# Optimization experiments

Hardware: AMD Instinct MI355X
Metric: run time of the kernel (lower is better)

Reference implementation:

```python
import jax, jax.numpy as jnp
import numpy as np

H = 768
NH = 12
HD = H // NH
NDIM = 5
LN_EPS = 1e-5


def setup_inputs() -> dict:
    key = jax.random.key(0)
    ks = jax.random.split(key, 12)
    B, S = 4, 2048
    xavier = lambda k: jax.random.uniform(k, (H, H), jnp.float32, -1.0, 1.0) * np.sqrt(6.0 / (H + H))
    return {
        "hidden_states": jax.random.normal(ks[0], (B, S, H), jnp.float32),
        "Wq": xavier(ks[1]), "bq": jnp.zeros((H,), jnp.float32),
        "Wk": xavier(ks[2]), "bk": jnp.zeros((H,), jnp.float32),
        "Wv": xavier(ks[3]), "bv": jnp.zeros((H,), jnp.float32),
        "Wo": xavier(ks[4]), "bo": jnp.zeros((H,), jnp.float32),
        # per-dimension, per-head scalar biases (torch init: zeros; use small randn so grads are non-trivial)
        "dim_biases": 0.02 * jax.random.normal(ks[5], (NDIM, NH), jnp.float32),
        "ln_gamma": jnp.ones((H,), jnp.float32),
        "ln_beta": jnp.zeros((H,), jnp.float32),
        "attention_mask": jax.random.randint(ks[6], (4, 2048), 0, 2, jnp.int32),
        "dimension_idx": 2,
    }


def reference(hidden_states, Wq, bq, Wk, bk, Wv, bv, Wo, bo, dim_biases,
              ln_gamma, ln_beta, attention_mask, dimension_idx):
    B, S, _ = hidden_states.shape
    residual = hidden_states
    # torch nn.Linear: x @ W.T + b
    q = (hidden_states @ Wq.T + bq).reshape(B, S, NH, HD).transpose(0, 2, 1, 3)  # [B,NH,S,HD]
    k = (hidden_states @ Wk.T + bk).reshape(B, S, NH, HD).transpose(0, 2, 1, 3)
    v = (hidden_states @ Wv.T + bv).reshape(B, S, NH, HD).transpose(0, 2, 1, 3)

    scores = jnp.einsum("bhqd,bhkd->bhqk", q, k) / np.sqrt(HD)  # [B,NH,S,S]
    if dimension_idx is not None and dimension_idx < NDIM:
        scores = scores + dim_biases[dimension_idx][None, :, None, None]
    # mask over key positions, broadcast over heads and queries
    scores = jnp.where(attention_mask[:, None, None, :] == 0, -jnp.inf, scores)
    attn = jax.nn.softmax(scores, axis=-1)

    ctx = jnp.einsum("bhqk,bhkd->bhqd", attn, v)  # [B,NH,S,HD]
    ctx = ctx.transpose(0, 2, 1, 3).reshape(B, S, H)
    out = ctx @ Wo.T + bo

    y = out + residual
    mu = jnp.mean(y, axis=-1, keepdims=True)
    var = jnp.var(y, axis=-1, keepdims=True)
    y = (y - mu) / jnp.sqrt(var + LN_EPS) * ln_gamma + ln_beta
    return y
```

## Files before the change

kernel.cpp:

```cpp
#include <hip/hip_runtime.h>
#include <hip/hip_bf16.h>

#define HH    768
#define NHEAD 12
#define HDIM  64
#define BB    4
#define SS    2048
#define MM    (BB*SS)
#define NDIMS 5
#define WEL   (HH*HH)
#define LOG2E 1.44269504088896f
#define QSCALE 0.180336881f

typedef unsigned short u16;
typedef __attribute__((ext_vector_type(8))) short short8;
typedef __attribute__((ext_vector_type(4))) float floatx4;
typedef __attribute__((ext_vector_type(16))) float floatx16;
typedef __attribute__((ext_vector_type(4))) unsigned int uint4v;
typedef __attribute__((ext_vector_type(2))) unsigned int uint2v;

__device__ __forceinline__ float bf2f(u16 u) {
    return __uint_as_float(((unsigned int)u) << 16);
}
__device__ __forceinline__ u16 f2bf(float f) {
    unsigned int x = __float_as_uint(f);
    unsigned int r = (x + 0x7fffu + ((x >> 16) & 1u)) >> 16;
    return (u16)r;
}
__device__ __forceinline__ unsigned int pack_bf16x2(float a, float b) {
    float2 f2 = make_float2(a, b);
    __hip_bfloat162 h2 = __float22bfloat162_rn(f2);
    return *reinterpret_cast<unsigned int*>(&h2);
}
__device__ __forceinline__ void gld16(const u16* g, u16* l) {
    __builtin_amdgcn_global_load_lds(
        (const __attribute__((address_space(1))) unsigned int*)g,
        (__attribute__((address_space(3))) unsigned int*)l, 16, 0, 0);
}

__global__ __launch_bounds__(256) void f32_to_bf16(
    const float* __restrict__ in, u16* __restrict__ out, int n8)
{
    int i = blockIdx.x * 256 + threadIdx.x;
    if (i >= n8) return;
    float4 a = ((const float4*)in)[i*2];
    float4 b = ((const float4*)in)[i*2 + 1];
    ushort4 lo, hi;
    lo.x = f2bf(a.x); lo.y = f2bf(a.y); lo.z = f2bf(a.z); lo.w = f2bf(a.w);
    hi.x = f2bf(b.x); hi.y = f2bf(b.y); hi.z = f2bf(b.z); hi.w = f2bf(b.w);
    ((ushort4*)out)[i*2]     = lo;
    ((ushort4*)out)[i*2 + 1] = hi;
}

#define XCVT_BLKS ((MM*HH)/8/256)
#define WCVT_BLKS (WEL/8/256)
__global__ __launch_bounds__(256) void cvt_all(
    const float* __restrict__ x,
    const float* __restrict__ W0, const float* __restrict__ W1,
    const float* __restrict__ W2, const float* __restrict__ W3,
    u16* __restrict__ xb, u16* __restrict__ wb)
{
    const int bid = blockIdx.x;
    const float* src;
    u16* dst;
    int i;
    if (bid < XCVT_BLKS) {
        src = x; dst = xb; i = bid * 256 + threadIdx.x;
    } else {
        const int wsel = (bid - XCVT_BLKS) / WCVT_BLKS;
        src = (wsel == 0) ? W0 : (wsel == 1) ? W1 : (wsel == 2) ? W2 : W3;
        dst = wb + (size_t)wsel * WEL;
        i = ((bid - XCVT_BLKS) % WCVT_BLKS) * 256 + threadIdx.x;
    }
    float4 a = ((const float4*)src)[i*2];
    float4 b = ((const float4*)src)[i*2 + 1];
    ushort4 lo, hi;
    lo.x = f2bf(a.x); lo.y = f2bf(a.y); lo.z = f2bf(a.z); lo.w = f2bf(a.w);
    hi.x = f2bf(b.x); hi.y = f2bf(b.y); hi.z = f2bf(b.z); hi.w = f2bf(b.w);
    ((ushort4*)dst)[i*2]     = lo;
    ((ushort4*)dst)[i*2 + 1] = hi;
}

__global__ __launch_bounds__(256) void v_transpose(
    const u16* __restrict__ V, u16* __restrict__ vt)
{
    __shared__ unsigned Ls[64][36];
    const int t = threadIdx.x;
    const int kt = blockIdx.x, h = blockIdx.y, b = blockIdx.z;
    const int p  = t & 31;
    const int dg = (t >> 5) * 8;
    const u16* va = V + ((size_t)(b*SS + kt*64 + 2*p))*HH + h*HDIM + dg;
    const u16* vb = va + HH;
    uint4 A = *(const uint4*)va;
    uint4 Bv = *(const uint4*)vb;
    const unsigned* Aw = (const unsigned*)&A;
    const unsigned* Bw = (const unsigned*)&Bv;
    #pragma unroll
    for (int i = 0; i < 4; ++i) {
        unsigned a = Aw[i], c = Bw[i];
        Ls[dg + 2*i][p]     = (a & 0xffffu) | (c << 16);
        Ls[dg + 2*i + 1][p] = (a >> 16) | (c & 0xffff0000u);
    }
    __syncthreads();
    const int d = t >> 2, kc = (t & 3) * 8;
    uint4 o0 = *(const uint4*)&Ls[d][kc];
    uint4 o1 = *(const uint4*)&Ls[d][kc + 4];
    u16* dst = vt + ((size_t)((b*NHEAD + h)*HDIM + d))*SS + kt*64 + kc*2;
    *(uint4*)dst       = o0;
    *(uint4*)(dst + 8) = o1;
}

__global__ __launch_bounds__(256, 3) void gemm_gld_qkv(
    const u16* __restrict__ Xb, const u16* __restrict__ Wb3,
    const float* __restrict__ bq, const float* __restrict__ bk, const float* __restrict__ bv,
    u16* __restrict__ oq, u16* __restrict__ ok, u16* __restrict__ ov)
{
    __shared__ u16 Xs[128][64];
    __shared__ u16 Ws[192][64];
    const int t = threadIdx.x;
    const int w = t >> 6, lane = t & 63;
    const int wy = w >> 1, wx = w & 1;
    const int m = lane & 31, hh = lane >> 5;
    const int grow = lane >> 3;
    const int cg   = (lane & 7) ^ grow;

    const int flat = blockIdx.x + 12 * blockIdx.y;
    const int swz  = (flat & 7) * 96 + (flat >> 3);
    const int j0 = (swz % 12) * 192;
    const int i0 = (swz / 12) * 128;
    const int sel = j0 / HH;
    const int lj  = j0 - sel * HH;
    const float* biasL = ((sel == 0) ? bq : (sel == 1) ? bk : bv) + lj;
    u16* outL = ((sel == 0) ? oq : (sel == 1) ? ok : ov) + lj;
    const u16* Wrows = Wb3 + (size_t)j0 * HH;

    floatx16 acc[2][3];
    #pragma unroll
    for (int am = 0; am < 2; ++am)
        #pragma unroll
        for (int bn = 0; bn < 3; ++bn)
            #pragma unroll
            for (int r = 0; r < 16; ++r) acc[am][bn][r] = 0.f;

    for (int k0 = 0; k0 < HH; k0 += 64) {
        __syncthreads();
        #pragma unroll
        for (int j = 0; j < 4; ++j) {
            const int r = w*32 + j*8;
            gld16(Xb + (size_t)(i0 + r + grow)*HH + k0 + cg*8, &Xs[r][0]);
        }
        #pragma unroll
        for (int j = 0; j < 6; ++j) {
            const int r = w*48 + j*8;
            gld16(Wrows + (size_t)(r + grow)*HH + k0 + cg*8, &Ws[r][0]);
        }
        __syncthreads();

        #pragma unroll
        for (int kh = 0; kh < 4; ++kh) {
            const int ch = kh*2 + hh;
            short8 af[2], bf[3];
            #pragma unroll
            for (int am = 0; am < 2; ++am) {
                const int row = wy*64 + am*32 + m;
                af[am] = *(const short8*)&Xs[row][(ch ^ (m & 7))*8];
            }
            #pragma unroll
            for (int bn = 0; bn < 3; ++bn) {
                const int row = wx*96 + bn*32 + m;
                bf[bn] = *(const short8*)&Ws[row][(ch ^ (m & 7))*8];
            }
            #pragma unroll
            for (int am = 0; am < 2; ++am)
                #pragma unroll
                for (int bn = 0; bn < 3; ++bn)
                    acc[am][bn] = __builtin_amdgcn_mfma_f32_32x32x16_bf16(
                        af[am], bf[bn], acc[am][bn], 0, 0, 0);
        }
    }

    float bb[3];
    #pragma unroll
    for (int bn = 0; bn < 3; ++bn) bb[bn] = biasL[wx*96 + bn*32 + m];
    #pragma unroll
    for (int am = 0; am < 2; ++am)
        #pragma unroll
        for (int bn = 0; bn < 3; ++bn)
            #pragma unroll
            for (int r = 0; r < 16; ++r) {
                int row = i0 + wy*64 + am*32 + (r & 3) + 8*(r >> 2) + 4*hh;
                outL[(size_t)row*HH + wx*96 + bn*32 + m] = f2bf(acc[am][bn][r] + bb[bn]);
            }
}

__global__ __launch_bounds__(256) void gemm_gld_m64(
    const u16* __restrict__ Xb, const u16* __restrict__ Wb,
    const float* __restrict__ bias, u16* __restrict__ out)
{
    __shared__ u16 Xs[64][64];
    __shared__ u16 Ws[128][64];
    const int t = threadIdx.x;
    const int w = t >> 6, lane = t & 63;
    const int m = lane & 31, hh = lane >> 5;
    const int grow = lane >> 3;
    const int cg   = (lane & 7) ^ grow;

    const int flat = blockIdx.x + 6 * blockIdx.y;
    const int swz  = (flat & 7) * 96 + (flat >> 3);
    const int j0 = (swz % 6) * 128;
    const int i0 = (swz / 6) * 64;

    floatx16 acc[2];
    #pragma unroll
    for (int am = 0; am < 2; ++am)
        #pragma unroll
        for (int r = 0; r < 16; ++r) acc[am][r] = 0.f;

    for (int k0 = 0; k0 < HH; k0 += 64) {
        __syncthreads();
        #pragma unroll
        for (int j = 0; j < 2; ++j) {
            const int r = w*16 + j*8;
            gld16(Xb + (size_t)(i0 + r + grow)*HH + k0 + cg*8, &Xs[r][0]);
        }
        #pragma unroll
        for (int j = 0; j < 4; ++j) {
            const int r = w*32 + j*8;
            gld16(Wb + (size_t)(j0 + r + grow)*HH + k0 + cg*8, &Ws[r][0]);
        }
        __syncthreads();

        #pragma unroll
        for (int kh = 0; kh < 4; ++kh) {
            const int ch = kh*2 + hh;
            short8 af[2], bf;
            af[0] = *(const short8*)&Xs[m][(ch ^ (m & 7))*8];
            af[1] = *(const short8*)&Xs[32 + m][(ch ^ (m & 7))*8];
            bf    = *(const short8*)&Ws[w*32 + m][(ch ^ (m & 7))*8];
            acc[0] = __builtin_amdgcn_mfma_f32_32x32x16_bf16(af[0], bf, acc[0], 0, 0, 0);
            acc[1] = __builtin_amdgcn_mfma_f32_32x32x16_bf16(af[1], bf, acc[1], 0, 0, 0);
        }
    }

    const float bb = bias[j0 + w*32 + m];
    #pragma unroll
    for (int am = 0; am < 2; ++am)
        #pragma unroll
        for (int r = 0; r < 16; ++r) {
            int row = i0 + am*32 + (r & 3) + 8*(r >> 2) + 4*hh;
            out[(size_t)row*HH + j0 + w*32 + m] = f2bf(acc[am][r] + bb);
        }
}

__global__ __launch_bounds__(256) void gemm_mfma_nt(
    const u16* __restrict__ Xb, const float* __restrict__ W,
    const float* __restrict__ bias, u16* __restrict__ out)
{
    __shared__ u16 Xs[128][40];
    __shared__ u16 Wt[64][40];
    const int t = threadIdx.x;
    const int w = t >> 6, lane = t & 63;
    const int c = lane & 15, qd = lane >> 4;
    const int i0 = blockIdx.y * 128, j0 = blockIdx.x * 64;
    const int xrow = t >> 1, xoff = (t & 1) * 16;
    const int wn = t >> 2, woff = (t & 3) * 8;

    floatx4 acc[2][4];
    #pragma unroll
    for (int mt = 0; mt < 2; ++mt)
        #pragma unroll
        for (int nt = 0; nt < 4; ++nt) acc[mt][nt] = (floatx4){0.f,0.f,0.f,0.f};

    for (int k0 = 0; k0 < HH; k0 += 32) {
        uint4 xa  = *(const uint4*)(Xb + (size_t)(i0 + xrow)*HH + k0 + xoff);
        uint4 xb2 = *(const uint4*)(Xb + (size_t)(i0 + xrow)*HH + k0 + xoff + 8);
        float4 wa = *(const float4*)(W + (size_t)(j0 + wn)*HH + k0 + woff);
        float4 wb = *(const float4*)(W + (size_t)(j0 + wn)*HH + k0 + woff + 4);
        __syncthreads();
        *(uint4*)&Xs[xrow][xoff]     = xa;
        *(uint4*)&Xs[xrow][xoff + 8] = xb2;
        ushort4 w0, w1;
        w0.x = f2bf(wa.x); w0.y = f2bf(wa.y); w0.z = f2bf(wa.z); w0.w = f2bf(wa.w);
        w1.x = f2bf(wb.x); w1.y = f2bf(wb.y); w1.z = f2bf(wb.z); w1.w = f2bf(wb.w);
        *(ushort4*)&Wt[wn][woff]     = w0;
        *(ushort4*)&Wt[wn][woff + 4] = w1;
        __syncthreads();

        short8 a0 = *(const short8*)&Xs[w*32 + c][qd*8];
        short8 a1 = *(const short8*)&Xs[w*32 + 16 + c][qd*8];
        #pragma unroll
        for (int nt = 0; nt < 4; ++nt) {
            short8 bfr = *(const short8*)&Wt[nt*16 + c][qd*8];
            acc[0][nt] = __builtin_amdgcn_mfma_f32_16x16x32_bf16(a0, bfr, acc[0][nt], 0, 0, 0);
            acc[1][nt] = __builtin_amdgcn_mfma_f32_16x16x32_bf16(a1, bfr, acc[1][nt], 0, 0, 0);
        }
    }

    float bv[4];
    #pragma unroll
    for (int nt = 0; nt < 4; ++nt) bv[nt] = bias[j0 + nt*16 + c];
    #pragma unroll
    for (int mt = 0; mt < 2; ++mt)
        #pragma unroll
        for (int nt = 0; nt < 4; ++nt)
            #pragma unroll
            for (int r = 0; r < 4; ++r)
                out[(size_t)(i0 + w*32 + mt*16 + qd*4 + r)*HH + j0 + nt*16 + c] =
                    f2bf(acc[mt][nt][r] + bv[nt]);
}

__global__ __launch_bounds__(256, 3) void attn_mfma32(
    const u16* __restrict__ Q, const u16* __restrict__ K, const u16* __restrict__ vt,
    const float* __restrict__ dim_biases, const int* __restrict__ mask,
    const int* __restrict__ dim_idx_p, u16* __restrict__ ctx)
{
    __shared__ u16 Ks[2][64][64];
    __shared__ u16 Vs[2][64][64];
    __shared__ float madd[2][64];

    const int t = threadIdx.x;
    const int w = t >> 6, lane = t & 63;
    const int ql = lane & 31, hi = lane >> 5;
    const int sw7 = ql & 7;

    const int flat = blockIdx.x + 16 * (blockIdx.y + 12 * blockIdx.z);
    const int swz  = (flat & 7) * 96 + (flat >> 3);
    const int q0 = (swz & 15) * 128;
    const int h  = (swz >> 4) % NHEAD;
    const int b  = swz / (16 * NHEAD);

    const int didx = *dim_idx_p;
    const float db2 = ((didx < NDIMS) ? dim_biases[didx*NHEAD + h] : 0.f) * LOG2E;

    const int grow = lane >> 3;
    const int cg   = (lane & 7) ^ grow;

    const u16* Vrows = vt + (size_t)(b*NHEAD + h)*HDIM*SS;

    short8 ones;
    #pragma unroll
    for (int j = 0; j < 8; ++j) ones[j] = (short)0x3F80;

    short8 qv[4];
    {
        const u16* qsrc = Q + ((size_t)(b*SS + q0 + w*32 + ql))*HH + h*HDIM + 8*hi;
        #pragma unroll
        for (int s = 0; s < 4; ++s) {
            ushort4 u0 = *(const ushort4*)(qsrc + s*16);
            ushort4 u1 = *(const ushort4*)(qsrc + s*16 + 4);
            const u16 uu[8] = {u0.x,u0.y,u0.z,u0.w,u1.x,u1.y,u1.z,u1.w};
            #pragma unroll
            for (int j = 0; j < 8; ++j)
                qv[s][j] = (short)f2bf(bf2f(uu[j]) * QSCALE);
        }
    }

    floatx16 o[2], lacc;
    #pragma unroll
    for (int r = 0; r < 16; ++r) { o[0][r] = 0.f; o[1][r] = 0.f; lacc[r] = 0.f; }

    int mreg = 0;

    auto issueKV = [&](int kt, int buf) {
        #pragma unroll
        for (int j = 0; j < 2; ++j) {
            const int rbase = w*16 + j*8;
            gld16(K + (size_t)(b*SS + kt*64 + rbase + grow)*HH + h*HDIM + cg*8,
                  &Ks[buf][rbase][0]);
            gld16(Vrows + (size_t)(rbase + grow)*SS + kt*64 + cg*8,
                  &Vs[buf][rbase][0]);
        }
    };
    auto issueM = [&](int kt) {
        if (t < 64) mreg = mask[(size_t)b*SS + kt*64 + t];
    };
    auto writeM = [&](int buf) {
        if (t < 64) madd[buf][t] = (mreg != 0) ? db2 : -1e30f;
    };

    issueKV(0, 0);
    issueM(0);
    writeM(0);

    for (int kt = 0; kt < SS/64; ++kt) {
        const int cur = kt & 1;
        __syncthreads();
        const bool more = (kt + 1 < SS/64);
        if (more) { issueKV(kt + 1, cur ^ 1); issueM(kt + 1); }

        #pragma unroll
        for (int kblk = 0; kblk < 2; ++kblk) {
            const u16* kb = &Ks[cur][kblk*32 + ql][0];

            floatx16 z;
            #pragma unroll
            for (int qq = 0; qq < 4; ++qq) {
                float4 mv = *(const float4*)&madd[cur][kblk*32 + qq*8 + 4*hi];
                z[qq*4+0] = mv.x; z[qq*4+1] = mv.y; z[qq*4+2] = mv.z; z[qq*4+3] = mv.w;
            }
            short8 kf[4];
            #pragma unroll
            for (int s = 0; s < 4; ++s)
                kf[s] = *(const short8*)(kb + ((s*2 + hi) ^ sw7)*8);
            __builtin_amdgcn_s_setprio(1);
            #pragma unroll
            for (int s = 0; s < 4; ++s)
                z = __builtin_amdgcn_mfma_f32_32x32x16_bf16(kf[s], qv[s], z, 0, 0, 0);
            __builtin_amdgcn_s_setprio(0);

            #pragma unroll
            for (int r = 0; r < 16; ++r) z[r] = __builtin_amdgcn_exp2f(z[r]);

            #pragma unroll
            for (int ks = 0; ks < 2; ++ks) {
                unsigned x0 = pack_bf16x2(z[ks*8 + 0], z[ks*8 + 1]);
                unsigned y0 = pack_bf16x2(z[ks*8 + 4], z[ks*8 + 5]);
                unsigned x1 = pack_bf16x2(z[ks*8 + 2], z[ks*8 + 3]);
                unsigned y1 = pack_bf16x2(z[ks*8 + 6], z[ks*8 + 7]);
                uint2v s0 = __builtin_amdgcn_permlane32_swap(x0, y0, false, false);
                uint2v s1 = __builtin_amdgcn_permlane32_swap(x1, y1, false, false);
                uint4v pv; pv[0] = s0[0]; pv[1] = s1[0]; pv[2] = s0[1]; pv[3] = s1[1];
                short8 pa = __builtin_bit_cast(short8, pv);

                const int ck = kblk*4 + ks*2 + hi;
                short8 vf0 = *(const short8*)&Vs[cur][ql][(ck ^ sw7)*8];
                short8 vf1 = *(const short8*)&Vs[cur][32 + ql][(ck ^ sw7)*8];

                __builtin_amdgcn_s_setprio(1);
                lacc = __builtin_amdgcn_mfma_f32_32x32x16_bf16(pa, ones, lacc, 0, 0, 0);
                o[0] = __builtin_amdgcn_mfma_f32_32x32x16_bf16(pa, vf0, o[0], 0, 0, 0);
                o[1] = __builtin_amdgcn_mfma_f32_32x32x16_bf16(pa, vf1, o[1], 0, 0, 0);
                __builtin_amdgcn_s_setprio(0);
            }
        }

        if (more) writeM(cur ^ 1);
    }

    #pragma unroll
    for (int r = 0; r < 16; ++r) {
        float l = lacc[r];
        float inv = (l > 0.f) ? 1.f / l : 0.f;
        const int qrow = q0 + w*32 + (r & 3) + 8*(r >> 2) + 4*hi;
        u16* dst = ctx + ((size_t)(b*SS + qrow))*HH + h*HDIM + ql;
        dst[0]  = f2bf(o[0][r] * inv);
        dst[32] = f2bf(o[1][r] * inv);
    }
}

__global__ __launch_bounds__(256) void add_ln_wave(
    const u16* __restrict__ proj, const float* __restrict__ resid,
    const float* __restrict__ gamma, const float* __restrict__ beta,
    float* __restrict__ out)
{
    const int t = threadIdx.x, w = t >> 6, lane = t & 63;
    const int row = blockIdx.x * 4 + w;
    const size_t base = (size_t)row * HH + lane * 12;
    const int gbase = lane * 12;

    float x[12];
    #pragma unroll
    for (int j = 0; j < 3; ++j) {
        ushort4 p = *(const ushort4*)(proj + base + j*4);
        float4  r = *(const float4*)(resid + base + j*4);
        x[j*4+0] = bf2f(p.x) + r.x;
        x[j*4+1] = bf2f(p.y) + r.y;
        x[j*4+2] = bf2f(p.z) + r.z;
        x[j*4+3] = bf2f(p.w) + r.w;
    }
    float s = 0.f, ss = 0.f;
    #pragma unroll
    for (int j = 0; j < 12; ++j) { s += x[j]; ss += x[j]*x[j]; }
    #pragma unroll
    for (int off = 1; off < 64; off <<= 1) {
        s  += __shfl_xor(s, off);
        ss += __shfl_xor(ss, off);
    }
    float mean = s * (1.f/768.f);
    float var  = ss * (1.f/768.f) - mean*mean;
    float rstd = rsqrtf(fmaxf(var, 0.f) + 1e-5f);
    #pragma unroll
    for (int j = 0; j < 3; ++j) {
        float4 g = *(const float4*)(gamma + gbase + j*4);
        float4 bt = *(const float4*)(beta + gbase + j*4);
        float4 y;
        y.x = (x[j*4+0]-mean)*rstd*g.x + bt.x;
        y.y = (x[j*4+1]-mean)*rstd*g.y + bt.y;
        y.z = (x[j*4+2]-mean)*rstd*g.z + bt.z;
        y.w = (x[j*4+3]-mean)*rstd*g.w + bt.w;
        *(float4*)(out + base + j*4) = y;
    }
}

extern "C" void kernel_launch(void* const* d_in, const int* in_sizes, int n_in,
                              void* d_out, int out_size, void* d_ws, size_t ws_size,
                              hipStream_t stream)
{
    (void)in_sizes; (void)n_in; (void)out_size;
    const float* x    = (const float*)d_in[0];
    const float* Wq   = (const float*)d_in[1];
    const float* bq   = (const float*)d_in[2];
    const float* Wk   = (const float*)d_in[3];
    const float* bk   = (const float*)d_in[4];
    const float* Wv   = (const float*)d_in[5];
    const float* bv   = (const float*)d_in[6];
    const float* Wo   = (const float*)d_in[7];
    const float* bo   = (const float*)d_in[8];
    const float* dimb = (const float*)d_in[9];
    const float* gam  = (const float*)d_in[10];
    const float* bet  = (const float*)d_in[11];
    const int* mask   = (const int*)d_in[12];
    const int* didx   = (const int*)d_in[13];

    const size_t N = (size_t)MM * HH;
    if (ws_size < 4 * N * sizeof(u16)) return;
    u16* ws = (u16*)d_ws;
    u16* q    = ws;
    u16* kbuf = ws + N;
    u16* vbuf = ws + 2*N;
    u16* slot3 = ws + 3*N;
    u16* xb   = slot3;
    u16* vtb  = slot3;
    u16* ctx  = vbuf;
    u16* proj = q;

    const bool bigws = ws_size >= (4 * N + 4 * (size_t)WEL) * sizeof(u16);
    u16* wb = ws + 4 * N;

    if (bigws) {
        cvt_all<<<XCVT_BLKS + 4*WCVT_BLKS, 256, 0, stream>>>(x, Wq, Wk, Wv, Wo, xb, wb);
        gemm_gld_qkv<<<dim3(3*HH/192, MM/128), 256, 0, stream>>>(
            xb, wb, bq, bk, bv, q, kbuf, vbuf);
    } else {
        f32_to_bf16<<<(int)(N/8/256), 256, 0, stream>>>(x, xb, (int)(N/8));
        dim3 gg(HH/64, MM/128);
        gemm_mfma_nt<<<gg, 256, 0, stream>>>(xb, Wq, bq, q);
        gemm_mfma_nt<<<gg, 256, 0, stream>>>(xb, Wk, bk, kbuf);
        gemm_mfma_nt<<<gg, 256, 0, stream>>>(xb, Wv, bv, vbuf);
    }
    v_transpose<<<dim3(SS/64, NHEAD, BB), 256, 0, stream>>>(vbuf, vtb);
    attn_mfma32<<<dim3(SS/128, NHEAD, BB), 256, 0, stream>>>(q, kbuf, vtb, dimb, mask, didx, ctx);
    if (bigws) gemm_gld_m64<<<dim3(HH/128, MM/64), 256, 0, stream>>>(ctx, wb + 3*WEL, bo, proj);
    else {
        dim3 gg(HH/64, MM/128);
        gemm_mfma_nt<<<gg, 256, 0, stream>>>(ctx, Wo, bo, proj);
    }
    add_ln_wave<<<MM/4, 256, 0, stream>>>(proj, x, gam, bet, (float*)d_out);
}
```

Before: 242.5 us.

## Fuse V transpose into QKV GEMM epilogue by computing transposed V tiles

```diff
diff --git a/kernel.cpp b/kernel.cpp
--- a/kernel.cpp
+++ b/kernel.cpp
@@ -113,7 +113,7 @@
 __global__ __launch_bounds__(256, 3) void gemm_gld_qkv(
     const u16* __restrict__ Xb, const u16* __restrict__ Wb3,
     const float* __restrict__ bq, const float* __restrict__ bk, const float* __restrict__ bv,
-    u16* __restrict__ oq, u16* __restrict__ ok, u16* __restrict__ ov)
+    u16* __restrict__ oq, u16* __restrict__ ok, u16* __restrict__ vt)
 {
     __shared__ u16 Xs[128][64];
     __shared__ u16 Ws[192][64];
@@ -131,7 +131,6 @@
     const int sel = j0 / HH;
     const int lj  = j0 - sel * HH;
     const float* biasL = ((sel == 0) ? bq : (sel == 1) ? bk : bv) + lj;
-    u16* outL = ((sel == 0) ? oq : (sel == 1) ? ok : ov) + lj;
     const u16* Wrows = Wb3 + (size_t)j0 * HH;
 
     floatx16 acc[2][3];
@@ -142,55 +141,106 @@
             #pragma unroll
             for (int r = 0; r < 16; ++r) acc[am][bn][r] = 0.f;
 
-    for (int k0 = 0; k0 < HH; k0 += 64) {
-        __syncthreads();
-        #pragma unroll
-        for (int j = 0; j < 4; ++j) {
-            const int r = w*32 + j*8;
-            gld16(Xb + (size_t)(i0 + r + grow)*HH + k0 + cg*8, &Xs[r][0]);
-        }
-        #pragma unroll
-        for (int j = 0; j < 6; ++j) {
-            const int r = w*48 + j*8;
-            gld16(Wrows + (size_t)(r + grow)*HH + k0 + cg*8, &Ws[r][0]);
-        }
-        __syncthreads();
-
-        #pragma unroll
-        for (int kh = 0; kh < 4; ++kh) {
-            const int ch = kh*2 + hh;
-            short8 af[2], bf[3];
-            #pragma unroll
-            for (int am = 0; am < 2; ++am) {
-                const int row = wy*64 + am*32 + m;
-                af[am] = *(const short8*)&Xs[row][(ch ^ (m & 7))*8];
-            }
-            #pragma unroll
-            for (int bn = 0; bn < 3; ++bn) {
-                const int row = wx*96 + bn*32 + m;
-                bf[bn] = *(const short8*)&Ws[row][(ch ^ (m & 7))*8];
-            }
-            #pragma unroll
-            for (int am = 0; am < 2; ++am)
+    if (sel != 2) {
+        for (int k0 = 0; k0 < HH; k0 += 64) {
+            __syncthreads();
+            #pragma unroll
+            for (int j = 0; j < 4; ++j) {
+                const int r = w*32 + j*8;
+                gld16(Xb + (size_t)(i0 + r + grow)*HH + k0 + cg*8, &Xs[r][0]);
+            }
+            #pragma unroll
+            for (int j = 0; j < 6; ++j) {
+                const int r = w*48 + j*8;
+                gld16(Wrows + (size_t)(r + grow)*HH + k0 + cg*8, &Ws[r][0]);
+            }
+            __syncthreads();
+
+            #pragma unroll
+            for (int kh = 0; kh < 4; ++kh) {
+                const int ch = kh*2 + hh;
+                short8 af[2], bf[3];
+                #pragma unroll
+                for (int am = 0; am < 2; ++am)
+                    af[am] = *(const short8*)&Xs[wy*64 + am*32 + m][(ch ^ (m & 7))*8];
                 #pragma unroll
                 for (int bn = 0; bn < 3; ++bn)
-                    acc[am][bn] = __builtin_amdgcn_mfma_f32_32x32x16_bf16(
-                        af[am], bf[bn], acc[am][bn], 0, 0, 0);
-        }
-    }
-
-    float bb[3];
-    #pragma unroll
-    for (int bn = 0; bn < 3; ++bn) bb[bn] = biasL[wx*96 + bn*32 + m];
-    #pragma unroll
-    for (int am = 0; am < 2; ++am)
-        #pragma unroll
-        for (int bn = 0; bn < 3; ++bn)
-            #pragma unroll
-            for (int r = 0; r < 16; ++r) {
-                int row = i0 + wy*64 + am*32 + (r & 3) + 8*(r >> 2) + 4*hh;
-                outL[(size_t)row*HH + wx*96 + bn*32 + m] = f2bf(acc[am][bn][r] + bb[bn]);
-            }
+                    bf[bn] = *(const short8*)&Ws[wx*96 + bn*32 + m][(ch ^ (m & 7))*8];
+                #pragma unroll
+                for (int am = 0; am < 2; ++am)
+                    #pragma unroll
+                    for (int bn = 0; bn < 3; ++bn)
+                        acc[am][bn] = __builtin_amdgcn_mfma_f32_32x32x16_bf16(
+                            af[am], bf[bn], acc[am][bn], 0, 0, 0);
+            }
+        }
+
+        u16* outL = ((sel == 0) ? oq : ok) + lj;
+        float bb[3];
+        #pragma unroll
+        for (int bn = 0; bn < 3; ++bn) bb[bn] = biasL[wx*96 + bn*32 + m];
+        #pragma unroll
+        for (int am = 0; am < 2; ++am)
+            #pragma unroll
+            for (int bn = 0; bn < 3; ++bn)
+                #pragma unroll
+                for (int r = 0; r < 16; ++r) {
+                    int row = i0 + wy*64 + am*32 + (r & 3) + 8*(r >> 2) + 4*hh;
+                    outL[(size_t)row*HH + wx*96 + bn*32 + m] = f2bf(acc[am][bn][r] + bb[bn]);
+                }
+    } else {
+        for (int k0 = 0; k0 < HH; k0 += 64) {
+            __syncthreads();
+            #pragma unroll
+            for (int j = 0; j < 4; ++j) {
+                const int r = w*32 + j*8;
+                gld16(Xb + (size_t)(i0 + r + grow)*HH + k0 + cg*8, &Xs[r][0]);
+            }
+            #pragma unroll
+            for (int j = 0; j < 6; ++j) {
+                const int r = w*48 + j*8;
+                gld16(Wrows + (size_t)(r + grow)*HH + k0 + cg*8, &Ws[r][0]);
+            }
+            __syncthreads();
+
+            #pragma unroll
+            for (int kh = 0; kh < 4; ++kh) {
+                const int ch = kh*2 + hh;
+                short8 af[2], bf[3];
+                #pragma unroll
+                for (int am = 0; am < 2; ++am)
+                    af[am] = *(const short8*)&Xs[wy*64 + am*32 + m][(ch ^ (m & 7))*8];
+                #pragma unroll
+                for (int bn = 0; bn < 3; ++bn)
+                    bf[bn] = *(const short8*)&Ws[wx*96 + bn*32 + m][(ch ^ (m & 7))*8];
+                #pragma unroll
+                for (int am = 0; am < 2; ++am)
+                    #pragma unroll
+                    for (int bn = 0; bn < 3; ++bn)
+                        acc[am][bn] = __builtin_amdgcn_mfma_f32_32x32x16_bf16(
+                            bf[bn], af[am], acc[am][bn], 0, 0, 0);
+            }
+        }
+
+        const int b_ = i0 / SS;
+        const int key0 = (i0 % SS) + wy*64 + m;
+        #pragma unroll
+        for (int am = 0; am < 2; ++am)
+            #pragma unroll
+            for (int bn = 0; bn < 3; ++bn)
+                #pragma unroll
+                for (int qq = 0; qq < 4; ++qq) {
+                    float4 bv4 = *(const float4*)&biasL[wx*96 + bn*32 + qq*8 + 4*hh];
+                    const float* bvp = (const float*)&bv4;
+                    #pragma unroll
+                    for (int j = 0; j < 4; ++j) {
+                        const int r = qq*4 + j;
+                        const int wcol = wx*96 + bn*32 + qq*8 + 4*hh + j;
+                        vt[(size_t)(b_*HH + lj + wcol)*SS + key0 + am*32] =
+                            f2bf(acc[am][bn][r] + bvp[j]);
+                    }
+                }
+    }
 }
 
 __global__ __launch_bounds__(256) void gemm_gld_m64(
@@ -517,11 +567,10 @@
     u16* ws = (u16*)d_ws;
     u16* q    = ws;
     u16* kbuf = ws + N;
-    u16* vbuf = ws + 2*N;
+    u16* vtb  = ws + 2*N;
     u16* slot3 = ws + 3*N;
     u16* xb   = slot3;
-    u16* vtb  = slot3;
-    u16* ctx  = vbuf;
+    u16* ctx  = slot3;
     u16* proj = q;
 
     const bool bigws = ws_size >= (4 * N + 4 * (size_t)WEL) * sizeof(u16);
@@ -530,20 +579,18 @@
     if (bigws) {
         cvt_all<<<XCVT_BLKS + 4*WCVT_BLKS, 256, 0, stream>>>(x, Wq, Wk, Wv, Wo, xb, wb);
         gemm_gld_qkv<<<dim3(3*HH/192, MM/128), 256, 0, stream>>>(
-            xb, wb, bq, bk, bv, q, kbuf, vbuf);
+            xb, wb, bq, bk, bv, q, kbuf, vtb);
+        attn_mfma32<<<dim3(SS/128, NHEAD, BB), 256, 0, stream>>>(q, kbuf, vtb, dimb, mask, didx, ctx);
+        gemm_gld_m64<<<dim3(HH/128, MM/64), 256, 0, stream>>>(ctx, wb + 3*WEL, bo, proj);
     } else {
         f32_to_bf16<<<(int)(N/8/256), 256, 0, stream>>>(x, xb, (int)(N/8));
         dim3 gg(HH/64, MM/128);
         gemm_mfma_nt<<<gg, 256, 0, stream>>>(xb, Wq, bq, q);
         gemm_mfma_nt<<<gg, 256, 0, stream>>>(xb, Wk, bk, kbuf);
-        gemm_mfma_nt<<<gg, 256, 0, stream>>>(xb, Wv, bv, vbuf);
-    }
-    v_transpose<<<dim3(SS/64, NHEAD, BB), 256, 0, stream>>>(vbuf, vtb);
-    attn_mfma32<<<dim3(SS/128, NHEAD, BB), 256, 0, stream>>>(q, kbuf, vtb, dimb, mask, didx, ctx);
-    if (bigws) gemm_gld_m64<<<dim3(HH/128, MM/64), 256, 0, stream>>>(ctx, wb + 3*WEL, bo, proj);
-    else {
-        dim3 gg(HH/64, MM/128);
-        gemm_mfma_nt<<<gg, 256, 0, stream>>>(ctx, Wo, bo, proj);
+        gemm_mfma_nt<<<gg, 256, 0, stream>>>(xb, Wv, bv, vtb);
+        v_transpose<<<dim3(SS/64, NHEAD, BB), 256, 0, stream>>>(vtb, slot3);
+        attn_mfma32<<<dim3(SS/128, NHEAD, BB), 256, 0, stream>>>(q, kbuf, slot3, dimb, mask, didx, vtb);
+        gemm_mfma_nt<<<dim3(HH/64, MM/128), 256, 0, stream>>>(vtb, Wo, bo, proj);
     }
     add_ln_wave<<<MM/4, 256, 0, stream>>>(proj, x, gam, bet, (float*)d_out);
 }
```

After: 237.0 us. 1.02x faster.
